# Kernel optimization log

Hardware: AMD Instinct MI355X
Metric: run time of the kernel (lower is better)

The kernel has to match this reference:

```python
import jax, jax.numpy as jnp
import numpy as np

NUM_ITERATIONS = 3


def squash(t, axis=-1):
    # scale * t / ||t|| with scale = ||t||^2 / (1 + ||t||^2)
    sq = jnp.sum(t * t, axis=axis, keepdims=True)
    scale = sq / (1.0 + sq)
    return scale * t / jnp.sqrt(sq)


def setup_inputs() -> dict:
    key = jax.random.key(0)
    k1, k2 = jax.random.split(key)
    B, N, Ci = 256, 1152, 8   # batch, num_route_nodes, in_channels
    C, Co = 10, 16            # num_capsules, out_channels
    x = jax.random.normal(k1, (B, N, Ci), dtype=jnp.float32)
    route_weights = jax.random.normal(k2, (C, N, Ci, Co), dtype=jnp.float32)
    return {"x": x, "route_weights": route_weights}


def reference(x, route_weights):
    # priors: [C, B, N, 1, Co] (matches x[None,:,:,None,:] @ W[:,None])
    priors = jnp.einsum('bni,cnio->cbno', x, route_weights)[:, :, :, None, :]
    logits = jnp.zeros_like(priors)
    outputs = None
    for i in range(NUM_ITERATIONS):
        probs = jax.nn.softmax(logits, axis=2)  # softmax over route nodes (dim=2)
        outputs = squash(jnp.sum(probs * priors, axis=2, keepdims=True))  # [C,B,1,1,Co]
        if i != NUM_ITERATIONS - 1:
            # agreement: [C,B,N,1,1], broadcasts into logits
            logits = logits + jnp.sum(priors * outputs, axis=-1, keepdims=True)
    return outputs
```

## Files before the change

kernel.cpp:

```cpp
#include <hip/hip_runtime.h>
#include <hip/hip_fp16.h>

#define NB     384
#define ROWS   3
#define N_ROUTE 1152
#define RB     18
#define NCHUNK 16

typedef __fp16 half2v __attribute__((ext_vector_type(2)));

__device__ __forceinline__ float fdot2u(unsigned int a, unsigned int b, float c) {
#if __has_builtin(__builtin_amdgcn_fdot2)
    half2v ha, hb;
    __builtin_memcpy(&ha, &a, 4);
    __builtin_memcpy(&hb, &b, 4);
    return __builtin_amdgcn_fdot2(ha, hb, c, false);
#else
    const __half2 h_a = *reinterpret_cast<const __half2*>(&a);
    const __half2 h_b = *reinterpret_cast<const __half2*>(&b);
    return fmaf(__low2float(h_a), __low2float(h_b),
           fmaf(__high2float(h_a), __high2float(h_b), c));
#endif
}

__device__ __forceinline__ unsigned int pkh(float a, float b) {
    half2v h = __builtin_amdgcn_cvt_pkrtz(a, b);
    unsigned int u;
    __builtin_memcpy(&u, &h, 4);
    return u;
}

template<int CTRL>
__device__ __forceinline__ float dpp_add(float v) {
    int t = __builtin_amdgcn_update_dpp(0, __float_as_int(v), CTRL, 0xF, 0xF, true);
    return v + __int_as_float(t);
}
__device__ __forceinline__ float wave_sum63(float v) {
    v = dpp_add<0x111>(v);
    v = dpp_add<0x112>(v);
    v = dpp_add<0x114>(v);
    v = dpp_add<0x118>(v);
    v = dpp_add<0x142>(v);
    v = dpp_add<0x143>(v);
    return v;
}

__global__ __launch_bounds__(256, 2)
void convert_w(const float* __restrict__ W, uint4* __restrict__ Wh)
{
    const int tid = blockIdx.x * 256 + threadIdx.x;
    const int c = tid / N_ROUTE;
    const int n = tid - c * N_ROUTE;
    const float* __restrict__ src = W + (size_t)tid * 128;
    unsigned int ch[16][4];
    #pragma unroll
    for (int ip = 0; ip < 4; ++ip) {
        float a[16], bb[16];
        #pragma unroll
        for (int q = 0; q < 4; ++q) {
            const float4 va = *reinterpret_cast<const float4*>(src + (2*ip)   * 16 + q*4);
            const float4 vb = *reinterpret_cast<const float4*>(src + (2*ip+1) * 16 + q*4);
            a[q*4+0]=va.x;  a[q*4+1]=va.y;  a[q*4+2]=va.z;  a[q*4+3]=va.w;
            bb[q*4+0]=vb.x; bb[q*4+1]=vb.y; bb[q*4+2]=vb.z; bb[q*4+3]=vb.w;
        }
        #pragma unroll
        for (int o = 0; o < 16; ++o) ch[o][ip] = pkh(a[o], bb[o]);
    }
    const int r = n >> 6, l = n & 63;
    uint4* __restrict__ dst = Wh + ((size_t)(c * RB + r) * NCHUNK) * 64 + l;
    #pragma unroll
    for (int o = 0; o < 16; ++o)
        dst[o * 64] = make_uint4(ch[o][0], ch[o][1], ch[o][2], ch[o][3]);
}

__global__ __launch_bounds__(NB, 2)
void capsule_routing_reg(const float* __restrict__ x,
                         const uint4* __restrict__ Wh,
                         float* __restrict__ out)
{
    __shared__ float red[6][20];
    __shared__ float vfin[16];

    const int t    = threadIdx.x;
    const int bid  = blockIdx.x;
    const int c    = bid >> 8;
    const int b    = bid & 255;
    const int lane = t & 63;
    const int wid  = t >> 6;

    unsigned int p2[ROWS][8];
    {
        const float* __restrict__ xb = x + (size_t)b * (N_ROUTE * 8);
        const uint4* __restrict__ Wc = Wh + (size_t)c * RB * NCHUNK * 64;
        #pragma unroll
        for (int k = 0; k < ROWS; ++k) {
            const int r = wid + 6 * k;
            const int n = (r << 6) + lane;
            const float4 x0 = *reinterpret_cast<const float4*>(xb + n * 8);
            const float4 x1 = *reinterpret_cast<const float4*>(xb + n * 8 + 4);
            const unsigned int xh[4] = { pkh(x0.x, x0.y), pkh(x0.z, x0.w),
                                         pkh(x1.x, x1.y), pkh(x1.z, x1.w) };
            const uint4* __restrict__ wr = Wc + (size_t)r * NCHUNK * 64 + lane;
            #pragma unroll
            for (int j = 0; j < 8; ++j) {
                const uint4 w0 = wr[(2 * j)     * 64];
                const uint4 w1 = wr[(2 * j + 1) * 64];
                float d0 = fdot2u(xh[0], w0.x, 0.f);
                d0 = fdot2u(xh[1], w0.y, d0);
                d0 = fdot2u(xh[2], w0.z, d0);
                d0 = fdot2u(xh[3], w0.w, d0);
                float d1 = fdot2u(xh[0], w1.x, 0.f);
                d1 = fdot2u(xh[1], w1.y, d1);
                d1 = fdot2u(xh[2], w1.z, d1);
                d1 = fdot2u(xh[3], w1.w, d1);
                p2[k][j] = pkh(d0, d1);
            }
        }
    }

    float lg[ROWS] = {0.f, 0.f, 0.f};
    unsigned int vph[8] = {0, 0, 0, 0, 0, 0, 0, 0};

    #pragma unroll
    for (int it = 0; it < 3; ++it) {
        float sp[16];
        #pragma unroll
        for (int o = 0; o < 16; ++o) sp[o] = 0.f;
        float zp = (it == 0) ? (float)ROWS : 0.f;

        #pragma unroll
        for (int k = 0; k < ROWS; ++k) {
            float e;
            if (it == 0) {
                e = 1.f;
            } else {
                float d = 0.f;
                #pragma unroll
                for (int j = 0; j < 8; ++j) d = fdot2u(p2[k][j], vph[j], d);
                lg[k] += d;
                e = __expf(lg[k]);
                zp += e;
            }
            #pragma unroll
            for (int j = 0; j < 8; ++j) {
                const __half2 h = *reinterpret_cast<const __half2*>(&p2[k][j]);
                sp[2 * j]     = fmaf(e, __low2float(h),  sp[2 * j]);
                sp[2 * j + 1] = fmaf(e, __high2float(h), sp[2 * j + 1]);
            }
        }

        #pragma unroll
        for (int o = 0; o < 16; ++o) sp[o] = wave_sum63(sp[o]);
        zp = wave_sum63(zp);
        if (lane == 63) {
            #pragma unroll
            for (int o = 0; o < 16; ++o) red[wid][o] = sp[o];
            red[wid][16] = zp;
        }
        __syncthreads();

        if (t < 16) {
            float tot = 0.f, Zt = 0.f;
            #pragma unroll
            for (int w2 = 0; w2 < 6; ++w2) {
                tot += red[w2][t];
                Zt  += red[w2][16];
            }
            const float so = tot / Zt;
            float sq = so * so;
            #pragma unroll
            for (int off = 8; off >= 1; off >>= 1) sq += __shfl_xor(sq, off);
            const float fac = sqrtf(sq) / (1.f + sq);
            const float vo  = so * fac;
            if (it == 2) out[((size_t)bid << 4) + t] = vo;
            else         vfin[t] = vo;
        }
        if (it < 2) {
            __syncthreads();
            const float4 v0 = *reinterpret_cast<const float4*>(&vfin[0]);
            const float4 v1 = *reinterpret_cast<const float4*>(&vfin[4]);
            const float4 v2 = *reinterpret_cast<const float4*>(&vfin[8]);
            const float4 v3 = *reinterpret_cast<const float4*>(&vfin[12]);
            vph[0] = pkh(v0.x, v0.y);  vph[1] = pkh(v0.z, v0.w);
            vph[2] = pkh(v1.x, v1.y);  vph[3] = pkh(v1.z, v1.w);
            vph[4] = pkh(v2.x, v2.y);  vph[5] = pkh(v2.z, v2.w);
            vph[6] = pkh(v3.x, v3.y);  vph[7] = pkh(v3.z, v3.w);
        }
    }
}

__global__ __launch_bounds__(NB, 2)
void capsule_routing_lds(const float* __restrict__ x,
                         const float* __restrict__ W,
                         float* __restrict__ out)
{
    __shared__ unsigned int P[N_ROUTE * 8];
    __shared__ float red[6][20];
    __shared__ float vfin[16];

    const int t    = threadIdx.x;
    const int bid  = blockIdx.x;
    const int c    = bid >> 8;
    const int b    = bid & 255;
    const int lane = t & 63;
    const int wid  = t >> 6;

    {
        const int og = t & 3;
        const int nl = t >> 2;
        const float* __restrict__ xb = x + (size_t)b * (N_ROUTE * 8);
        const float* __restrict__ Wc = W + (size_t)c * (N_ROUTE * 128);
        #pragma unroll 2
        for (int pp = 0; pp < 12; ++pp) {
            const int n = pp * 96 + nl;
            const float4 x0 = *reinterpret_cast<const float4*>(xb + n * 8);
            const float4 x1 = *reinterpret_cast<const float4*>(xb + n * 8 + 4);
            const float xs[8] = {x0.x, x0.y, x0.z, x0.w, x1.x, x1.y, x1.z, x1.w};
            const float* __restrict__ wp = Wc + (size_t)n * 128 + (og << 2);
            float4 acc = make_float4(0.f, 0.f, 0.f, 0.f);
            #pragma unroll
            for (int i = 0; i < 8; ++i) {
                const float4 w = *reinterpret_cast<const float4*>(wp + i * 16);
                acc.x = fmaf(xs[i], w.x, acc.x);
                acc.y = fmaf(xs[i], w.y, acc.y);
                acc.z = fmaf(xs[i], w.z, acc.z);
                acc.w = fmaf(xs[i], w.w, acc.w);
            }
            const int s    = (n >> 2) & 7;
            const int base = n << 3;
            P[base + (((og << 1)    ) ^ s)] = pkh(acc.x, acc.y);
            P[base + (((og << 1) + 1) ^ s)] = pkh(acc.z, acc.w);
        }
    }
    __syncthreads();

    float vprev[16];
    #pragma unroll
    for (int o = 0; o < 16; ++o) vprev[o] = 0.f;
    float lg[ROWS] = {0.f, 0.f, 0.f};

    #pragma unroll
    for (int it = 0; it < 3; ++it) {
        float sp[16];
        #pragma unroll
        for (int o = 0; o < 16; ++o) sp[o] = 0.f;
        float zp = (it == 0) ? (float)ROWS : 0.f;

        #pragma unroll
        for (int k = 0; k < ROWS; ++k) {
            const int n = t + k * NB;
            const int s = (n >> 2) & 7;
            const unsigned int* __restrict__ pr = &P[n << 3];
            __half2 h[8];
            #pragma unroll
            for (int j = 0; j < 8; ++j) {
                const unsigned int w = pr[j ^ s];
                h[j] = *reinterpret_cast<const __half2*>(&w);
            }
            float e;
            if (it == 0) {
                e = 1.f;
            } else {
                float d = 0.f;
                #pragma unroll
                for (int j = 0; j < 8; ++j) {
                    d = fmaf(__low2float(h[j]),  vprev[2 * j],     d);
                    d = fmaf(__high2float(h[j]), vprev[2 * j + 1], d);
                }
                lg[k] += d;
                e = __expf(lg[k]);
                zp += e;
            }
            #pragma unroll
            for (int j = 0; j < 8; ++j) {
                sp[2 * j]     = fmaf(e, __low2float(h[j]),  sp[2 * j]);
                sp[2 * j + 1] = fmaf(e, __high2float(h[j]), sp[2 * j + 1]);
            }
        }

        #pragma unroll
        for (int o = 0; o < 16; ++o) sp[o] = wave_sum63(sp[o]);
        zp = wave_sum63(zp);
        if (lane == 63) {
            #pragma unroll
            for (int o = 0; o < 16; ++o) red[wid][o] = sp[o];
            red[wid][16] = zp;
        }
        __syncthreads();

        if (t < 16) {
            float tot = 0.f, Zt = 0.f;
            #pragma unroll
            for (int w2 = 0; w2 < 6; ++w2) { tot += red[w2][t]; Zt += red[w2][16]; }
            const float so = tot / Zt;
            float sq = so * so;
            #pragma unroll
            for (int off = 8; off >= 1; off >>= 1) sq += __shfl_xor(sq, off);
            const float fac = sqrtf(sq) / (1.f + sq);
            const float vo  = so * fac;
            if (it == 2) out[((size_t)bid << 4) + t] = vo;
            else         vfin[t] = vo;
        }
        if (it < 2) {
            __syncthreads();
            #pragma unroll
            for (int o = 0; o < 16; ++o) vprev[o] = vfin[o];
        }
    }
}

extern "C" void kernel_launch(void* const* d_in, const int* in_sizes, int n_in,
                              void* d_out, int out_size, void* d_ws, size_t ws_size,
                              hipStream_t stream)
{
    const float* x   = (const float*)d_in[0];
    const float* W   = (const float*)d_in[1];
    float*       out = (float*)d_out;
    const size_t WH_BYTES = (size_t)10 * RB * NCHUNK * 64 * sizeof(uint4);

    if (ws_size >= WH_BYTES) {
        uint4* Wh = (uint4*)d_ws;
        convert_w<<<dim3(45), dim3(256), 0, stream>>>(W, Wh);
        capsule_routing_reg<<<dim3(10 * 256), dim3(NB), 0, stream>>>(x, Wh, out);
    } else {
        capsule_routing_lds<<<dim3(10 * 256), dim3(NB), 0, stream>>>(x, W, out);
    }
}
```

Before: 120.5 us.

## Process two batch rows per block to reuse W loads; parallelize W conversion

The routing kernel now handles two batch elements per block, so each loaded fp16 weight chunk feeds dot products for both batches. This halves W traffic and the block count, at the cost of doubled register state for priors and logits, which may pressure occupancy. The wave reduction now stops at 16-lane rows and writes four partials per wave to shared memory, cutting cross-row DPP steps in exchange for more LDS summation. The W conversion kernel is rewritten so each thread produces one uint4 from eight strided floats, using 720 blocks instead of 45 to spread the work across more of the GPU.

```diff
diff --git a/kernel.cpp b/kernel.cpp
--- a/kernel.cpp
+++ b/kernel.cpp
@@ -35,156 +35,170 @@
     int t = __builtin_amdgcn_update_dpp(0, __float_as_int(v), CTRL, 0xF, 0xF, true);
     return v + __int_as_float(t);
 }
-__device__ __forceinline__ float wave_sum63(float v) {
+__device__ __forceinline__ float wave_sum15(float v) {
     v = dpp_add<0x111>(v);
     v = dpp_add<0x112>(v);
     v = dpp_add<0x114>(v);
     v = dpp_add<0x118>(v);
-    v = dpp_add<0x142>(v);
-    v = dpp_add<0x143>(v);
     return v;
 }
 
-__global__ __launch_bounds__(256, 2)
+__global__ __launch_bounds__(256, 4)
 void convert_w(const float* __restrict__ W, uint4* __restrict__ Wh)
 {
-    const int tid = blockIdx.x * 256 + threadIdx.x;
-    const int c = tid / N_ROUTE;
-    const int n = tid - c * N_ROUTE;
-    const float* __restrict__ src = W + (size_t)tid * 128;
-    unsigned int ch[16][4];
+    const int tid  = blockIdx.x * 256 + threadIdx.x;
+    const int o    = tid & 15;
+    const int rest = tid >> 4;
+    const int l    = rest & 63;
+    const int cr   = rest >> 6;
+    const float* __restrict__ src = W + ((size_t)cr * 64 + l) * 128 + o;
+    float f[8];
     #pragma unroll
-    for (int ip = 0; ip < 4; ++ip) {
-        float a[16], bb[16];
-        #pragma unroll
-        for (int q = 0; q < 4; ++q) {
-            const float4 va = *reinterpret_cast<const float4*>(src + (2*ip)   * 16 + q*4);
-            const float4 vb = *reinterpret_cast<const float4*>(src + (2*ip+1) * 16 + q*4);
-            a[q*4+0]=va.x;  a[q*4+1]=va.y;  a[q*4+2]=va.z;  a[q*4+3]=va.w;
-            bb[q*4+0]=vb.x; bb[q*4+1]=vb.y; bb[q*4+2]=vb.z; bb[q*4+3]=vb.w;
-        }
-        #pragma unroll
-        for (int o = 0; o < 16; ++o) ch[o][ip] = pkh(a[o], bb[o]);
-    }
-    const int r = n >> 6, l = n & 63;
-    uint4* __restrict__ dst = Wh + ((size_t)(c * RB + r) * NCHUNK) * 64 + l;
-    #pragma unroll
-    for (int o = 0; o < 16; ++o)
-        dst[o * 64] = make_uint4(ch[o][0], ch[o][1], ch[o][2], ch[o][3]);
+    for (int i = 0; i < 8; ++i) f[i] = src[i * 16];
+    uint4 v;
+    v.x = pkh(f[0], f[1]);
+    v.y = pkh(f[2], f[3]);
+    v.z = pkh(f[4], f[5]);
+    v.w = pkh(f[6], f[7]);
+    Wh[((size_t)cr * 16 + o) * 64 + l] = v;
 }
 
 __global__ __launch_bounds__(NB, 2)
-void capsule_routing_reg(const float* __restrict__ x,
-                         const uint4* __restrict__ Wh,
-                         float* __restrict__ out)
+void capsule_routing_reg2(const float* __restrict__ x,
+                          const uint4* __restrict__ Wh,
+                          float* __restrict__ out)
 {
-    __shared__ float red[6][20];
-    __shared__ float vfin[16];
+    __shared__ float red[6][4][36];
+    __shared__ float vfin[2][16];
 
     const int t    = threadIdx.x;
-    const int bid  = blockIdx.x;
-    const int c    = bid >> 8;
-    const int b    = bid & 255;
     const int lane = t & 63;
     const int wid  = t >> 6;
-
-    unsigned int p2[ROWS][8];
+    const int bid  = blockIdx.x;
+    const int c    = bid >> 7;
+    const int b0   = (bid & 127) << 1;
+
+    unsigned int p2[2][ROWS][8];
     {
-        const float* __restrict__ xb = x + (size_t)b * (N_ROUTE * 8);
+        const float* __restrict__ xA = x + (size_t)b0 * (N_ROUTE * 8);
+        const float* __restrict__ xB = xA + N_ROUTE * 8;
         const uint4* __restrict__ Wc = Wh + (size_t)c * RB * NCHUNK * 64;
         #pragma unroll
         for (int k = 0; k < ROWS; ++k) {
             const int r = wid + 6 * k;
             const int n = (r << 6) + lane;
-            const float4 x0 = *reinterpret_cast<const float4*>(xb + n * 8);
-            const float4 x1 = *reinterpret_cast<const float4*>(xb + n * 8 + 4);
-            const unsigned int xh[4] = { pkh(x0.x, x0.y), pkh(x0.z, x0.w),
-                                         pkh(x1.x, x1.y), pkh(x1.z, x1.w) };
+            const float4 a0 = *reinterpret_cast<const float4*>(xA + n * 8);
+            const float4 a1 = *reinterpret_cast<const float4*>(xA + n * 8 + 4);
+            const float4 c0 = *reinterpret_cast<const float4*>(xB + n * 8);
+            const float4 c1 = *reinterpret_cast<const float4*>(xB + n * 8 + 4);
+            const unsigned int xhA[4] = { pkh(a0.x, a0.y), pkh(a0.z, a0.w),
+                                          pkh(a1.x, a1.y), pkh(a1.z, a1.w) };
+            const unsigned int xhB[4] = { pkh(c0.x, c0.y), pkh(c0.z, c0.w),
+                                          pkh(c1.x, c1.y), pkh(c1.z, c1.w) };
             const uint4* __restrict__ wr = Wc + (size_t)r * NCHUNK * 64 + lane;
             #pragma unroll
             for (int j = 0; j < 8; ++j) {
                 const uint4 w0 = wr[(2 * j)     * 64];
                 const uint4 w1 = wr[(2 * j + 1) * 64];
-                float d0 = fdot2u(xh[0], w0.x, 0.f);
-                d0 = fdot2u(xh[1], w0.y, d0);
-                d0 = fdot2u(xh[2], w0.z, d0);
-                d0 = fdot2u(xh[3], w0.w, d0);
-                float d1 = fdot2u(xh[0], w1.x, 0.f);
-                d1 = fdot2u(xh[1], w1.y, d1);
-                d1 = fdot2u(xh[2], w1.z, d1);
-                d1 = fdot2u(xh[3], w1.w, d1);
-                p2[k][j] = pkh(d0, d1);
-            }
-        }
-    }
-
-    float lg[ROWS] = {0.f, 0.f, 0.f};
-    unsigned int vph[8] = {0, 0, 0, 0, 0, 0, 0, 0};
+                float dA0 = fdot2u(xhA[0], w0.x, 0.f);
+                dA0 = fdot2u(xhA[1], w0.y, dA0);
+                dA0 = fdot2u(xhA[2], w0.z, dA0);
+                dA0 = fdot2u(xhA[3], w0.w, dA0);
+                float dA1 = fdot2u(xhA[0], w1.x, 0.f);
+                dA1 = fdot2u(xhA[1], w1.y, dA1);
+                dA1 = fdot2u(xhA[2], w1.z, dA1);
+                dA1 = fdot2u(xhA[3], w1.w, dA1);
+                float dB0 = fdot2u(xhB[0], w0.x, 0.f);
+                dB0 = fdot2u(xhB[1], w0.y, dB0);
+                dB0 = fdot2u(xhB[2], w0.z, dB0);
+                dB0 = fdot2u(xhB[3], w0.w, dB0);
+                float dB1 = fdot2u(xhB[0], w1.x, 0.f);
+                dB1 = fdot2u(xhB[1], w1.y, dB1);
+                dB1 = fdot2u(xhB[2], w1.z, dB1);
+                dB1 = fdot2u(xhB[3], w1.w, dB1);
+                p2[0][k][j] = pkh(dA0, dA1);
+                p2[1][k][j] = pkh(dB0, dB1);
+            }
+        }
+    }
+
+    float lg[2][ROWS] = {{0.f, 0.f, 0.f}, {0.f, 0.f, 0.f}};
+    unsigned int vph[2][8] = {{0,0,0,0,0,0,0,0}, {0,0,0,0,0,0,0,0}};
 
     #pragma unroll
     for (int it = 0; it < 3; ++it) {
-        float sp[16];
-        #pragma unroll
-        for (int o = 0; o < 16; ++o) sp[o] = 0.f;
-        float zp = (it == 0) ? (float)ROWS : 0.f;
-
-        #pragma unroll
-        for (int k = 0; k < ROWS; ++k) {
-            float e;
-            if (it == 0) {
-                e = 1.f;
-            } else {
-                float d = 0.f;
+        #pragma unroll
+        for (int bt = 0; bt < 2; ++bt) {
+            float sp[16];
+            #pragma unroll
+            for (int o = 0; o < 16; ++o) sp[o] = 0.f;
+            float zp = (it == 0) ? (float)ROWS : 0.f;
+
+            #pragma unroll
+            for (int k = 0; k < ROWS; ++k) {
+                float e;
+                if (it == 0) {
+                    e = 1.f;
+                } else {
+                    float d = 0.f;
+                    #pragma unroll
+                    for (int j = 0; j < 8; ++j) d = fdot2u(p2[bt][k][j], vph[bt][j], d);
+                    lg[bt][k] += d;
+                    e = __expf(lg[bt][k]);
+                    zp += e;
+                }
                 #pragma unroll
-                for (int j = 0; j < 8; ++j) d = fdot2u(p2[k][j], vph[j], d);
-                lg[k] += d;
-                e = __expf(lg[k]);
-                zp += e;
-            }
-            #pragma unroll
-            for (int j = 0; j < 8; ++j) {
-                const __half2 h = *reinterpret_cast<const __half2*>(&p2[k][j]);
-                sp[2 * j]     = fmaf(e, __low2float(h),  sp[2 * j]);
-                sp[2 * j + 1] = fmaf(e, __high2float(h), sp[2 * j + 1]);
-            }
-        }
-
-        #pragma unroll
-        for (int o = 0; o < 16; ++o) sp[o] = wave_sum63(sp[o]);
-        zp = wave_sum63(zp);
-        if (lane == 63) {
-            #pragma unroll
-            for (int o = 0; o < 16; ++o) red[wid][o] = sp[o];
-            red[wid][16] = zp;
+                for (int j = 0; j < 8; ++j) {
+                    const __half2 h = *reinterpret_cast<const __half2*>(&p2[bt][k][j]);
+                    sp[2 * j]     = fmaf(e, __low2float(h),  sp[2 * j]);
+                    sp[2 * j + 1] = fmaf(e, __high2float(h), sp[2 * j + 1]);
+                }
+            }
+
+            #pragma unroll
+            for (int o = 0; o < 16; ++o) sp[o] = wave_sum15(sp[o]);
+            zp = wave_sum15(zp);
+            if ((lane & 15) == 15) {
+                const int q = lane >> 4;
+                #pragma unroll
+                for (int o = 0; o < 16; ++o) red[wid][q][bt * 18 + o] = sp[o];
+                red[wid][q][bt * 18 + 16] = zp;
+            }
         }
         __syncthreads();
 
-        if (t < 16) {
+        if (t < 32) {
+            const int bt = t >> 4, o = t & 15;
             float tot = 0.f, Zt = 0.f;
             #pragma unroll
-            for (int w2 = 0; w2 < 6; ++w2) {
-                tot += red[w2][t];
-                Zt  += red[w2][16];
-            }
+            for (int w2 = 0; w2 < 6; ++w2)
+                #pragma unroll
+                for (int q = 0; q < 4; ++q) {
+                    tot += red[w2][q][bt * 18 + o];
+                    Zt  += red[w2][q][bt * 18 + 16];
+                }
             const float so = tot / Zt;
             float sq = so * so;
             #pragma unroll
-            for (int off = 8; off >= 1; off >>= 1) sq += __shfl_xor(sq, off);
+            for (int off = 8; off >= 1; off >>= 1) sq += __shfl_xor(sq, off, 16);
             const float fac = sqrtf(sq) / (1.f + sq);
             const float vo  = so * fac;
-            if (it == 2) out[((size_t)bid << 4) + t] = vo;
-            else         vfin[t] = vo;
+            if (it == 2) out[(((size_t)c << 8) + b0 + bt) * 16 + o] = vo;
+            else         vfin[bt][o] = vo;
         }
         if (it < 2) {
             __syncthreads();
-            const float4 v0 = *reinterpret_cast<const float4*>(&vfin[0]);
-            const float4 v1 = *reinterpret_cast<const float4*>(&vfin[4]);
-            const float4 v2 = *reinterpret_cast<const float4*>(&vfin[8]);
-            const float4 v3 = *reinterpret_cast<const float4*>(&vfin[12]);
-            vph[0] = pkh(v0.x, v0.y);  vph[1] = pkh(v0.z, v0.w);
-            vph[2] = pkh(v1.x, v1.y);  vph[3] = pkh(v1.z, v1.w);
-            vph[4] = pkh(v2.x, v2.y);  vph[5] = pkh(v2.z, v2.w);
-            vph[6] = pkh(v3.x, v3.y);  vph[7] = pkh(v3.z, v3.w);
+            #pragma unroll
+            for (int bt = 0; bt < 2; ++bt) {
+                const float4 v0 = *reinterpret_cast<const float4*>(&vfin[bt][0]);
+                const float4 v1 = *reinterpret_cast<const float4*>(&vfin[bt][4]);
+                const float4 v2 = *reinterpret_cast<const float4*>(&vfin[bt][8]);
+                const float4 v3 = *reinterpret_cast<const float4*>(&vfin[bt][12]);
+                vph[bt][0] = pkh(v0.x, v0.y);  vph[bt][1] = pkh(v0.z, v0.w);
+                vph[bt][2] = pkh(v1.x, v1.y);  vph[bt][3] = pkh(v1.z, v1.w);
+                vph[bt][4] = pkh(v2.x, v2.y);  vph[bt][5] = pkh(v2.z, v2.w);
+                vph[bt][6] = pkh(v3.x, v3.y);  vph[bt][7] = pkh(v3.z, v3.w);
+            }
         }
     }
 }
@@ -279,8 +293,18 @@
         }
 
         #pragma unroll
-        for (int o = 0; o < 16; ++o) sp[o] = wave_sum63(sp[o]);
-        zp = wave_sum63(zp);
+        for (int o = 0; o < 16; ++o) {
+            float v = wave_sum15(sp[o]);
+            v = dpp_add<0x142>(v);
+            v = dpp_add<0x143>(v);
+            sp[o] = v;
+        }
+        {
+            float v = wave_sum15(zp);
+            v = dpp_add<0x142>(v);
+            v = dpp_add<0x143>(v);
+            zp = v;
+        }
         if (lane == 63) {
             #pragma unroll
             for (int o = 0; o < 16; ++o) red[wid][o] = sp[o];
@@ -320,8 +344,8 @@
 
     if (ws_size >= WH_BYTES) {
         uint4* Wh = (uint4*)d_ws;
-        convert_w<<<dim3(45), dim3(256), 0, stream>>>(W, Wh);
-        capsule_routing_reg<<<dim3(10 * 256), dim3(NB), 0, stream>>>(x, Wh, out);
+        convert_w<<<dim3(720), dim3(256), 0, stream>>>(W, Wh);
+        capsule_routing_reg2<<<dim3(10 * 128), dim3(NB), 0, stream>>>(x, Wh, out);
     } else {
         capsule_routing_lds<<<dim3(10 * 256), dim3(NB), 0, stream>>>(x, W, out);
     }
```

Result: slower. 190.2 us (+57.9%).
